# Kernel tuning notes

Hardware: AMD Instinct MI355X
Metric: run time of the kernel (lower is better)

The kernel has to match this reference:

```python
import jax, jax.numpy as jnp
import numpy as np

# ---- static config (mirrors Spectral2xDown.__init__) ----
B, C_IN, C_OUT = 2, 256, 256
H_HI, W_HI = 256, 512
H_LO, W_LO = 128, 256
LMAX = H_LO            # 128
MMAX = W_LO // 2 + 1   # 129
GROUPS = 32
EPS_GN = 1e-5


def _cc_nodes_weights(n):
    """Clenshaw-Curtis nodes x_j=cos(pi*j/(n-1)) and quadrature weights on [-1,1]
    (torch_harmonics 'equiangular' grid)."""
    N = n - 1
    tj = np.pi * np.arange(n) / N
    xj = np.cos(tj)
    ks = np.arange(1, N // 2 + 1)
    b = np.where(2 * ks == N, 1.0, 2.0)
    s = (b / (4.0 * ks**2 - 1.0))[None, :] * np.cos(2.0 * ks[None, :] * tj[:, None])
    w = (2.0 / N) * (1.0 - s.sum(axis=1))
    w[0] = w[-1] = (1.0 / N**2) if (N % 2) else (1.0 / (N**2 - 1.0))
    return xj, w


def _legpoly(mmax, lmax, x):
    """Orthonormal associated Legendre (-1)^m c_lm P_lm(x), shape [mmax,lmax,len(x)]
    (torch_harmonics _precompute_legpoly, norm='ortho', csphase=True)."""
    nmax = max(mmax, lmax)
    vdm = np.zeros((nmax, nmax, len(x)))
    vdm[0, 0] = 1.0 / np.sqrt(4.0 * np.pi)
    for l in range(1, nmax):
        vdm[l - 1, l] = np.sqrt(2 * l + 1) * x * vdm[l - 1, l - 1]
        vdm[l, l] = np.sqrt((2 * l + 1) * (1 + x) * (1 - x) / (2 * l)) * vdm[l - 1, l - 1]
    for l in range(2, nmax):
        for m in range(0, l - 1):
            vdm[m, l] = (x * np.sqrt((2 * l - 1) / (l - m) * (2 * l + 1) / (l + m)) * vdm[m, l - 1]
                         - np.sqrt((l + m - 1) / (l - m) * (2 * l + 1) / (2 * l - 3)
                                   * (l - m - 1) / (l + m)) * vdm[m, l - 2])
    vdm = vdm[:mmax, :lmax].copy()
    for m in range(1, mmax, 2):  # Condon-Shortley phase
        vdm[m] *= -1.0
    return vdm


def _precompute():
    ct_hi, w_hi = _cc_nodes_weights(H_HI)
    pct_hi = _legpoly(MMAX, LMAX, np.flip(np.arccos(ct_hi)) * 0 + np.cos(np.flip(np.arccos(ct_hi))))
    wmat_hi = pct_hi * w_hi[None, None, :]          # quadrature folded in: [M,L,K_hi]
    ct_lo, _ = _cc_nodes_weights(H_LO)
    pct_lo = _legpoly(MMAX, LMAX, np.cos(np.flip(np.arccos(ct_lo))))  # [M,L,K_lo]
    return wmat_hi.astype(np.float32), pct_lo.astype(np.float32)


def setup_inputs() -> dict:
    key = jax.random.key(0)
    k1, k2 = jax.random.split(key, 2)
    x = jax.random.normal(k1, (B, C_IN, H_HI, W_HI), jnp.float32)
    conv_w = jax.random.normal(k2, (C_OUT, C_IN), jnp.float32) / np.sqrt(C_IN)
    conv_b = jnp.zeros((C_OUT,), jnp.float32)
    gamma = jnp.ones((C_OUT,), jnp.float32)
    beta = jnp.zeros((C_OUT,), jnp.float32)
    wmat_hi, pct_lo = _precompute()
    return {"x": x, "conv_w": conv_w, "conv_b": conv_b, "gamma": gamma, "beta": beta,
            "wmat_hi": jnp.asarray(wmat_hi), "pct_lo": jnp.asarray(pct_lo)}


def reference(x, conv_w, conv_b, gamma, beta, wmat_hi, pct_lo):
    # --- forward real SHT on high-res grid (2*pi * rfft(norm='forward') + Legendre quadrature) ---
    X = (2.0 * jnp.pi / W_HI) * jnp.fft.rfft(x, axis=-1)     # [B,C,K_hi,W_HI//2+1]
    X = X[..., :MMAX]                                        # truncate to mmax
    flm_r = jnp.einsum('bckm,mlk->bclm', X.real, wmat_hi)    # [B,C,L,M]
    flm_i = jnp.einsum('bckm,mlk->bclm', X.imag, wmat_hi)
    # --- inverse real SHT on low-res grid ---
    g = (jnp.einsum('bclm,mlk->bckm', flm_r, pct_lo)
         + 1j * jnp.einsum('bclm,mlk->bckm', flm_i, pct_lo))  # [B,C,K_lo,M]
    y = jnp.fft.irfft(g, n=W_LO, axis=-1) * W_LO             # irfft norm='forward'
    # --- 1x1 conv -> GroupNorm(32) -> exact GELU ---
    h = jnp.einsum('bchw,oc->bohw', y, conv_w) + conv_b[None, :, None, None]
    hg = h.reshape(B, GROUPS, C_OUT // GROUPS, H_LO, W_LO)
    mu = hg.mean(axis=(2, 3, 4), keepdims=True)
    var = ((hg - mu) ** 2).mean(axis=(2, 3, 4), keepdims=True)
    hn = ((hg - mu) * jax.lax.rsqrt(var + EPS_GN)).reshape(B, C_OUT, H_LO, W_LO)
    out = hn * gamma[None, :, None, None] + beta[None, :, None, None]
    return jax.nn.gelu(out, approximate=False)
```

## Files before the change

### kernel.cpp

```cpp
#include <hip/hip_runtime.h>
#include <math.h>


#define ROWS_HI 131072
#define ROWS_LO 65536

#define B_FT    0LL
#define B_FIT   262144LL
#define B_WM    393216LL
#define B_PCT   8781824LL
#define B_WB    12976128LL
#define B_STATS 13107200LL
#define B_R1    13107712LL
#define B_R2    80216576LL

typedef __attribute__((ext_vector_type(8))) short bf16x8;
typedef __attribute__((ext_vector_type(8))) unsigned short ushort8;
typedef __attribute__((ext_vector_type(4))) unsigned short ushort4v;
typedef __attribute__((ext_vector_type(4))) float f32x4;

__device__ inline unsigned short f2bf(float f){
  unsigned int u = __float_as_uint(f);
  unsigned int r = u + 0x7FFFu + ((u >> 16) & 1u);
  return (unsigned short)(r >> 16);
}

__global__ __launch_bounds__(256) void k_tables(unsigned char* __restrict__ ws){
  unsigned short* FT  = (unsigned short*)(ws + B_FT);
  unsigned short* FIT = (unsigned short*)(ws + B_FIT);
  float* stats = (float*)(ws + B_STATS);
  int idx = blockIdx.x*256 + threadIdx.x;
  if (idx < 131072){
    int p = idx >> 9, w = idx & 511, m = p >> 1;
    int pr = (m*w) & 511;
    float ang = (float)pr * (float)(2.0*M_PI/512.0);
    float s, c; sincosf(ang, &s, &c);
    const float S = (float)(2.0*M_PI/512.0);
    FT[idx] = f2bf((p & 1) ? (-S*s) : (S*c));
  }
  int i2 = idx - 131072;
  if (i2 >= 0 && i2 < 65536){
    int w = i2 >> 8, p = i2 & 255, m = p >> 1;
    float eps = (m == 0) ? 1.f : 2.f;
    int pr = (m*w) & 255;
    float ang = (float)pr * (float)(2.0*M_PI/256.0);
    float s, c; sincosf(ang, &s, &c);
    FIT[i2] = f2bf((p & 1) ? (-eps*s) : (eps*c));
  }
  int i3 = idx - (131072 + 65536);
  if (i3 >= 0 && i3 < 128) stats[i3] = 0.f;
}

__global__ __launch_bounds__(256) void k_prep(const float* __restrict__ wmat,
                                              const float* __restrict__ pct,
                                              const float* __restrict__ Wc,
                                              unsigned char* __restrict__ ws){
  unsigned short* WM = (unsigned short*)(ws + B_WM);
  unsigned short* PT = (unsigned short*)(ws + B_PCT);
  unsigned short* WB = (unsigned short*)(ws + B_WB);
  int idx = blockIdx.x*256 + threadIdx.x;
  if (idx < 4194304){
    WM[idx] = f2bf(wmat[idx]);
  } else if (idx < 6291456){
    int j = idx - 4194304;
    int m = j >> 14, kp = (j >> 7) & 127, l = j & 127;
    PT[j] = f2bf(pct[m*16384 + l*128 + kp]);
  } else if (idx < 6356992){
    int j = idx - 6291456;
    WB[j] = f2bf(Wc[j]);
  }
}

template<int AMODE, int CMODE, bool BIAS, int MT, int NT, int SKIP>
__global__ __launch_bounds__(256) void k_gemm(
    const float* __restrict__ Af,
    const unsigned short* __restrict__ Abf,
    const unsigned short* __restrict__ Bt,
    float* __restrict__ Cf,
    unsigned short* __restrict__ Cbf,
    const float* __restrict__ bias,
    int ldA, int ldB, int ldC, int ksteps,
    long long sA, long long sB, int bzsh, long long sC)
{
  constexpr int BM = MT*32;
  constexpr int BN = NT*32;
  __shared__ unsigned short As[BM][40];
  __shared__ unsigned short Bs[BN][40];
  const int tid = threadIdx.x;
  const int z = blockIdx.z;
  const int m = z >> 1;
  const long long offA = (long long)z * sA;
  const long long offB = (long long)(z >> bzsh) * sB;
  const long long offC = (long long)z * sC;
  const int row0 = blockIdx.x * BM;
  const int n0   = blockIdx.y * BN;
  const int lane = tid & 63;
  const int wv = tid >> 6;
  const int wm = wv >> 1, wn = wv & 1;
  const int fr = lane & 15, q = lane >> 4;

  f32x4 acc[MT][NT];
#pragma unroll
  for (int i=0;i<MT;++i)
#pragma unroll
    for (int j=0;j<NT;++j) acc[i][j] = (f32x4){0.f,0.f,0.f,0.f};

  int ks0 = (SKIP == 2) ? (m >> 5) : 0;
  for (int ks = ks0; ks < ksteps; ++ks){
    const int k0 = ks * 32;
    if (AMODE == 0){
      const int row = tid >> 1, half = tid & 1;
      const float* s = Af + offA + (long long)(row0 + row) * ldA + k0 + half*16;
      float vv[16];
      *(float4*)(vv+0)  = *(const float4*)(s+0);
      *(float4*)(vv+4)  = *(const float4*)(s+4);
      *(float4*)(vv+8)  = *(const float4*)(s+8);
      *(float4*)(vv+12) = *(const float4*)(s+12);
      ushort8 H0, H1;
#pragma unroll
      for (int j=0;j<8;++j){ H0[j] = f2bf(vv[j]); H1[j] = f2bf(vv[8+j]); }
      *(ushort8*)&As[row][half*16]   = H0;
      *(ushort8*)&As[row][half*16+8] = H1;
    } else if (BM == 256){
      const unsigned short* s = Abf + offA + (long long)(row0 + tid) * ldA + k0;
      *(ushort8*)&As[tid][0]  = *(const ushort8*)(s);
      *(ushort8*)&As[tid][8]  = *(const ushort8*)(s+8);
      *(ushort8*)&As[tid][16] = *(const ushort8*)(s+16);
      *(ushort8*)&As[tid][24] = *(const ushort8*)(s+24);
    } else {
      const int row = tid >> 1, half = tid & 1;
      const unsigned short* s = Abf + offA + (long long)(row0 + row) * ldA + k0 + half*16;
      *(ushort8*)&As[row][half*16]   = *(const ushort8*)(s);
      *(ushort8*)&As[row][half*16+8] = *(const ushort8*)(s+8);
    }
    if (BN == 256){
      const unsigned short* s = Bt + offB + (long long)(n0 + tid) * ldB + k0;
      *(ushort8*)&Bs[tid][0]  = *(const ushort8*)(s);
      *(ushort8*)&Bs[tid][8]  = *(const ushort8*)(s+8);
      *(ushort8*)&Bs[tid][16] = *(const ushort8*)(s+16);
      *(ushort8*)&Bs[tid][24] = *(const ushort8*)(s+24);
    } else {
      const int row = tid >> 1, half = tid & 1;
      const unsigned short* s = Bt + offB + (long long)(n0 + row) * ldB + k0 + half*16;
      *(ushort8*)&Bs[row][half*16]   = *(const ushort8*)(s);
      *(ushort8*)&Bs[row][half*16+8] = *(const ushort8*)(s+8);
    }
    __syncthreads();
    bf16x8 ah[MT];
#pragma unroll
    for (int mt=0;mt<MT;++mt)
      ah[mt] = *(const bf16x8*)&As[wm*(MT*16)+mt*16+fr][q*8];
#pragma unroll
    for (int nt=0;nt<NT;++nt){
      if (SKIP == 1 && (wn*(NT*16) + nt*16 + 16 <= m)) continue;
      bf16x8 bb = *(const bf16x8*)&Bs[wn*(NT*16)+nt*16+fr][q*8];
#pragma unroll
      for (int mt=0;mt<MT;++mt)
        acc[mt][nt] = __builtin_amdgcn_mfma_f32_16x16x32_bf16(ah[mt], bb, acc[mt][nt], 0,0,0);
    }
    __syncthreads();
  }

  if (CMODE == 0){
#pragma unroll
    for (int mt=0;mt<MT;++mt){
      int row = row0 + wm*(MT*16) + mt*16 + q*4;
      float bv0=0.f,bv1=0.f,bv2=0.f,bv3=0.f;
      if (BIAS){ bv0=bias[row]; bv1=bias[row+1]; bv2=bias[row+2]; bv3=bias[row+3]; }
#pragma unroll
      for (int nt=0;nt<NT;++nt){
        int col = n0 + wn*(NT*16) + nt*16 + fr;
        float* dst = Cf + offC + (long long)row * ldC + col;
        dst[0]                = acc[mt][nt][0] + bv0;
        dst[(long long)ldC]   = acc[mt][nt][1] + bv1;
        dst[(long long)ldC*2] = acc[mt][nt][2] + bv2;
        dst[(long long)ldC*3] = acc[mt][nt][3] + bv3;
      }
    }
  } else if (CMODE == 1){
#pragma unroll
    for (int nt=0;nt<NT;++nt){
      int colp = n0 + wn*(NT*16) + nt*16 + fr;
#pragma unroll
      for (int mt=0;mt<MT;++mt){
        int rowb = row0 + wm*(MT*16) + mt*16 + q*4;
        ushort4v h;
        h[0] = f2bf(acc[mt][nt][0]);
        h[1] = f2bf(acc[mt][nt][1]);
        h[2] = f2bf(acc[mt][nt][2]);
        h[3] = f2bf(acc[mt][nt][3]);
        *(ushort4v*)&Cbf[offC + (long long)colp * ldC + rowb] = h;
      }
    }
  } else {
#pragma unroll
    for (int mt=0;mt<MT;++mt){
      int row = row0 + wm*(MT*16) + mt*16 + q*4;
#pragma unroll
      for (int nt=0;nt<NT;++nt){
        int col = n0 + wn*(NT*16) + nt*16 + fr;
        unsigned short* dst = Cbf + offC + (long long)row * ldC + col;
        dst[0]      = f2bf(acc[mt][nt][0]);
        dst[ldC]    = f2bf(acc[mt][nt][1]);
        dst[ldC*2]  = f2bf(acc[mt][nt][2]);
        dst[ldC*3]  = f2bf(acc[mt][nt][3]);
      }
    }
  }
}

__global__ __launch_bounds__(256) void k_trb(const unsigned short* __restrict__ g,
                                             unsigned short* __restrict__ gT){
  __shared__ unsigned short t[64][68];
  const int r0 = blockIdx.x * 64;
  const int p0 = blockIdx.y * 64;
  const int tr = threadIdx.x & 15, tc = threadIdx.x >> 4;
#pragma unroll
  for (int i=0;i<4;++i){
    int pl = tc + i*16;
    ushort4v v = *(const ushort4v*)(g + (long long)(p0+pl)*ROWS_LO + r0 + tr*4);
    *(ushort4v*)&t[pl][tr*4] = v;
  }
  __syncthreads();
#pragma unroll
  for (int i=0;i<4;++i){
    int rl = tc + i*16;
    ushort4v w;
    w[0]=t[tr*4+0][rl]; w[1]=t[tr*4+1][rl]; w[2]=t[tr*4+2][rl]; w[3]=t[tr*4+3][rl];
    *(ushort4v*)(gT + (long long)(r0+rl)*256 + p0 + tr*4) = w;
  }
}

__global__ __launch_bounds__(256) void k_tr2(const float* __restrict__ y,
                                             unsigned short* __restrict__ yT){
  __shared__ float t[64][65];
  const int s0 = blockIdx.x * 64;
  const int c0 = blockIdx.y * 64;
  const int b  = blockIdx.z;
  const int tr = threadIdx.x & 15, tc = threadIdx.x >> 4;
#pragma unroll
  for (int i=0;i<4;++i){
    int cl = tc + i*16;
    float4 v = *(const float4*)(y + (long long)b*8388608 + (long long)(c0+cl)*32768 + s0 + tr*4);
    t[cl][tr*4+0]=v.x; t[cl][tr*4+1]=v.y; t[cl][tr*4+2]=v.z; t[cl][tr*4+3]=v.w;
  }
  __syncthreads();
#pragma unroll
  for (int i=0;i<4;++i){
    int sl = tc + i*16;
    ushort4v w;
    w[0]=f2bf(t[tr*4+0][sl]); w[1]=f2bf(t[tr*4+1][sl]);
    w[2]=f2bf(t[tr*4+2][sl]); w[3]=f2bf(t[tr*4+3][sl]);
    *(ushort4v*)(yT + (long long)b*8388608 + (long long)(s0+sl)*256 + c0 + tr*4) = w;
  }
}

__global__ __launch_bounds__(256) void k_stats(const float* __restrict__ h,
                                               float* __restrict__ stats){
  const int bg = blockIdx.y;
  const int j  = blockIdx.x;
  const int t  = threadIdx.x;
  const float* base = h + (long long)bg*262144 + j*8192;
  float s = 0.f, ss = 0.f;
#pragma unroll
  for (int i=0;i<8;++i){
    float4 v = *(const float4*)(base + i*1024 + t*4);
    s  += v.x + v.y + v.z + v.w;
    ss += v.x*v.x + v.y*v.y + v.z*v.z + v.w*v.w;
  }
#pragma unroll
  for (int off=32; off>0; off>>=1){
    s  += __shfl_down(s, off, 64);
    ss += __shfl_down(ss, off, 64);
  }
  __shared__ float red[8];
  int wid = t >> 6;
  if ((t & 63) == 0){ red[wid*2] = s; red[wid*2+1] = ss; }
  __syncthreads();
  if (t == 0){
    float S  = red[0]+red[2]+red[4]+red[6];
    float SS = red[1]+red[3]+red[5]+red[7];
    atomicAdd(&stats[bg*2+0], S);
    atomicAdd(&stats[bg*2+1], SS);
  }
}

__global__ __launch_bounds__(256) void k_norm(float* __restrict__ out,
                                              const float* __restrict__ stats,
                                              const float* __restrict__ gamma,
                                              const float* __restrict__ beta){
  long long idx4 = ((long long)blockIdx.x*256 + threadIdx.x)*4;
  int o = (int)((idx4 >> 15) & 255);
  int b = (int)(idx4 >> 23);
  int bg = b*32 + (o >> 3);
  const float inv_n = 1.0f/262144.0f;
  float mean = stats[bg*2+0] * inv_n;
  float var  = stats[bg*2+1] * inv_n - mean*mean;
  float sc = rsqrtf(var + 1e-5f);
  float ga = gamma[o], be = beta[o];
  float4 v = *(float4*)(out + idx4);
  float t0 = (v.x - mean)*sc*ga + be;
  float t1 = (v.y - mean)*sc*ga + be;
  float t2 = (v.z - mean)*sc*ga + be;
  float t3 = (v.w - mean)*sc*ga + be;
  const float ISQ2 = 0.70710678118654752f;
  v.x = 0.5f*t0*(1.0f + erff(t0*ISQ2));
  v.y = 0.5f*t1*(1.0f + erff(t1*ISQ2));
  v.z = 0.5f*t2*(1.0f + erff(t2*ISQ2));
  v.w = 0.5f*t3*(1.0f + erff(t3*ISQ2));
  *(float4*)(out + idx4) = v;
}

extern "C" void kernel_launch(void* const* d_in, const int* in_sizes, int n_in,
                              void* d_out, int out_size, void* d_ws, size_t ws_size,
                              hipStream_t stream){
  const float* x      = (const float*)d_in[0];
  const float* conv_w = (const float*)d_in[1];
  const float* conv_b = (const float*)d_in[2];
  const float* gamma  = (const float*)d_in[3];
  const float* beta   = (const float*)d_in[4];
  const float* wmat   = (const float*)d_in[5];
  const float* pct    = (const float*)d_in[6];
  unsigned char* ws = (unsigned char*)d_ws;

  unsigned short* FT   = (unsigned short*)(ws + B_FT);
  unsigned short* FIT  = (unsigned short*)(ws + B_FIT);
  unsigned short* WM   = (unsigned short*)(ws + B_WM);
  unsigned short* PT   = (unsigned short*)(ws + B_PCT);
  unsigned short* WB   = (unsigned short*)(ws + B_WB);
  float*          stats= (float*)(ws + B_STATS);
  unsigned short* Xbf  = (unsigned short*)(ws + B_R1);
  unsigned short* gb   = (unsigned short*)(ws + B_R1);
  float*          y    = (float*)(ws + B_R1);
  unsigned short* flmb = (unsigned short*)(ws + B_R2);
  unsigned short* gTb  = (unsigned short*)(ws + B_R2);
  unsigned short* yT   = (unsigned short*)(ws + B_R2);
  float* out = (float*)d_out;

  k_tables<<<769, 256, 0, stream>>>(ws);
  k_prep  <<<24832, 256, 0, stream>>>(wmat, pct, conv_w, ws);

  k_gemm<0,1,false,4,8,0><<<dim3(1024,1,1), 256, 0, stream>>>(
      x, nullptr, FT, nullptr, Xbf, nullptr, 512, 512, ROWS_HI, 16, 0, 0, 0, 0);
  k_gemm<1,2,false,4,4,1><<<dim3(4,1,256), 256, 0, stream>>>(
      nullptr, Xbf, WM, nullptr, flmb, nullptr, 256, 256, 128, 8,
      131072LL, 32768LL, 1, 65536LL);
  k_gemm<1,2,false,4,4,2><<<dim3(4,1,256), 256, 0, stream>>>(
      nullptr, flmb, PT, nullptr, gb, nullptr, 128, 128, 128, 4,
      65536LL, 16384LL, 1, 65536LL);
  k_trb<<<dim3(1024,4), 256, 0, stream>>>(gb, gTb);
  k_gemm<1,0,false,4,8,0><<<dim3(512,1,1), 256, 0, stream>>>(
      nullptr, gTb, FIT, y, nullptr, nullptr, 256, 256, 256, 8, 0, 0, 0, 0);
  k_tr2<<<dim3(512,4,2), 256, 0, stream>>>(y, yT);
  k_gemm<1,0,true,8,4,0><<<dim3(1,256,2), 256, 0, stream>>>(
      nullptr, WB, yT, out, nullptr, conv_b, 256, 256, 32768, 8,
      0, 8388608LL, 0, 8388608LL);

  k_stats<<<dim3(32,64), 256, 0, stream>>>(out, stats);
  k_norm <<<16384, 256, 0, stream>>>(out, stats, gamma, beta);
}
```

Measured before the change: 670.5 us.

## Unify GEMM tiling to 128x128x64, fuse GroupNorm stats, store irfft output as bf16

All GEMMs now share one 128x128 tile with a 64-wide K step, replacing the earlier per-call tile shapes, and the launch grids are adjusted to match. The GroupNorm sum and sum-of-squares reduction moves into the epilogue of the 1x1-conv GEMM using wave shuffles and atomics, which removes the separate stats kernel and its extra read of the output. The inverse-FFT GEMM now writes bf16 directly, so the transpose kernel moves half the bytes. Costs are more atomics, a different occupancy profile from the larger LDS tiles with launch_bounds(256,3), and the stats epilogue assuming each 16-row fragment spans exactly two groups.

```diff
diff --git a/kernel.cpp b/kernel.cpp
--- a/kernel.cpp
+++ b/kernel.cpp
@@ -1,4 +1,5 @@
 #include <hip/hip_runtime.h>
+#include <hip/hip_bf16.h>
 #include <math.h>
 
 
@@ -23,6 +24,11 @@
   unsigned int u = __float_as_uint(f);
   unsigned int r = u + 0x7FFFu + ((u >> 16) & 1u);
   return (unsigned short)(r >> 16);
+}
+__device__ inline unsigned int pk2bf(float a, float b){
+  unsigned int lo = (unsigned int)f2bf(a);
+  unsigned int hi = (unsigned int)f2bf(b);
+  return lo | (hi << 16);
 }
 
 __global__ __launch_bounds__(256) void k_tables(unsigned char* __restrict__ ws){
@@ -71,134 +77,155 @@
   }
 }
 
-template<int AMODE, int CMODE, bool BIAS, int MT, int NT, int SKIP>
-__global__ __launch_bounds__(256) void k_gemm(
+template<int AMODE, int CMODE, bool BIAS, int SKIP, bool STATS>
+__global__ __launch_bounds__(256, 3) void k_gemm(
     const float* __restrict__ Af,
     const unsigned short* __restrict__ Abf,
     const unsigned short* __restrict__ Bt,
     float* __restrict__ Cf,
     unsigned short* __restrict__ Cbf,
     const float* __restrict__ bias,
+    float* __restrict__ stats,
     int ldA, int ldB, int ldC, int ksteps,
     long long sA, long long sB, int bzsh, long long sC)
 {
-  constexpr int BM = MT*32;
-  constexpr int BN = NT*32;
-  __shared__ unsigned short As[BM][40];
-  __shared__ unsigned short Bs[BN][40];
+  __shared__ unsigned short As[128][80];
+  __shared__ unsigned short Bs[128][80];
   const int tid = threadIdx.x;
   const int z = blockIdx.z;
   const int m = z >> 1;
   const long long offA = (long long)z * sA;
   const long long offB = (long long)(z >> bzsh) * sB;
   const long long offC = (long long)z * sC;
-  const int row0 = blockIdx.x * BM;
-  const int n0   = blockIdx.y * BN;
+  const int row0 = blockIdx.x * 128;
+  const int n0   = blockIdx.y * 128;
   const int lane = tid & 63;
   const int wv = tid >> 6;
   const int wm = wv >> 1, wn = wv & 1;
   const int fr = lane & 15, q = lane >> 4;
-
-  f32x4 acc[MT][NT];
-#pragma unroll
-  for (int i=0;i<MT;++i)
-#pragma unroll
-    for (int j=0;j<NT;++j) acc[i][j] = (f32x4){0.f,0.f,0.f,0.f};
-
-  int ks0 = (SKIP == 2) ? (m >> 5) : 0;
+  const int srow = tid >> 1, shalf = tid & 1;
+
+  f32x4 acc[4][4];
+#pragma unroll
+  for (int i=0;i<4;++i)
+#pragma unroll
+    for (int j=0;j<4;++j) acc[i][j] = (f32x4){0.f,0.f,0.f,0.f};
+
+  const int ks0 = (SKIP == 2) ? (m >> 6) : 0;
   for (int ks = ks0; ks < ksteps; ++ks){
-    const int k0 = ks * 32;
+    const int k0 = ks * 64;
     if (AMODE == 0){
-      const int row = tid >> 1, half = tid & 1;
-      const float* s = Af + offA + (long long)(row0 + row) * ldA + k0 + half*16;
-      float vv[16];
-      *(float4*)(vv+0)  = *(const float4*)(s+0);
-      *(float4*)(vv+4)  = *(const float4*)(s+4);
-      *(float4*)(vv+8)  = *(const float4*)(s+8);
-      *(float4*)(vv+12) = *(const float4*)(s+12);
-      ushort8 H0, H1;
-#pragma unroll
-      for (int j=0;j<8;++j){ H0[j] = f2bf(vv[j]); H1[j] = f2bf(vv[8+j]); }
-      *(ushort8*)&As[row][half*16]   = H0;
-      *(ushort8*)&As[row][half*16+8] = H1;
-    } else if (BM == 256){
-      const unsigned short* s = Abf + offA + (long long)(row0 + tid) * ldA + k0;
-      *(ushort8*)&As[tid][0]  = *(const ushort8*)(s);
-      *(ushort8*)&As[tid][8]  = *(const ushort8*)(s+8);
-      *(ushort8*)&As[tid][16] = *(const ushort8*)(s+16);
-      *(ushort8*)&As[tid][24] = *(const ushort8*)(s+24);
+      const float* s = Af + offA + (long long)(row0 + srow) * ldA + k0 + shalf*32;
+#pragma unroll
+      for (int b2=0;b2<2;++b2){
+        float4 v0 = *(const float4*)(s + b2*16 + 0);
+        float4 v1 = *(const float4*)(s + b2*16 + 4);
+        float4 v2 = *(const float4*)(s + b2*16 + 8);
+        float4 v3 = *(const float4*)(s + b2*16 + 12);
+        unsigned int u0 = pk2bf(v0.x, v0.y), u1 = pk2bf(v0.z, v0.w);
+        unsigned int u2 = pk2bf(v1.x, v1.y), u3 = pk2bf(v1.z, v1.w);
+        unsigned int u4 = pk2bf(v2.x, v2.y), u5 = pk2bf(v2.z, v2.w);
+        unsigned int u6 = pk2bf(v3.x, v3.y), u7 = pk2bf(v3.z, v3.w);
+        unsigned int* d = (unsigned int*)&As[srow][shalf*32 + b2*16];
+        d[0]=u0; d[1]=u1; d[2]=u2; d[3]=u3; d[4]=u4; d[5]=u5; d[6]=u6; d[7]=u7;
+      }
     } else {
-      const int row = tid >> 1, half = tid & 1;
-      const unsigned short* s = Abf + offA + (long long)(row0 + row) * ldA + k0 + half*16;
-      *(ushort8*)&As[row][half*16]   = *(const ushort8*)(s);
-      *(ushort8*)&As[row][half*16+8] = *(const ushort8*)(s+8);
-    }
-    if (BN == 256){
-      const unsigned short* s = Bt + offB + (long long)(n0 + tid) * ldB + k0;
-      *(ushort8*)&Bs[tid][0]  = *(const ushort8*)(s);
-      *(ushort8*)&Bs[tid][8]  = *(const ushort8*)(s+8);
-      *(ushort8*)&Bs[tid][16] = *(const ushort8*)(s+16);
-      *(ushort8*)&Bs[tid][24] = *(const ushort8*)(s+24);
-    } else {
-      const int row = tid >> 1, half = tid & 1;
-      const unsigned short* s = Bt + offB + (long long)(n0 + row) * ldB + k0 + half*16;
-      *(ushort8*)&Bs[row][half*16]   = *(const ushort8*)(s);
-      *(ushort8*)&Bs[row][half*16+8] = *(const ushort8*)(s+8);
+      const unsigned short* s = Abf + offA + (long long)(row0 + srow) * ldA + k0 + shalf*32;
+      *(ushort8*)&As[srow][shalf*32]    = *(const ushort8*)(s);
+      *(ushort8*)&As[srow][shalf*32+8]  = *(const ushort8*)(s+8);
+      *(ushort8*)&As[srow][shalf*32+16] = *(const ushort8*)(s+16);
+      *(ushort8*)&As[srow][shalf*32+24] = *(const ushort8*)(s+24);
+    }
+    {
+      const unsigned short* s = Bt + offB + (long long)(n0 + srow) * ldB + k0 + shalf*32;
+      *(ushort8*)&Bs[srow][shalf*32]    = *(const ushort8*)(s);
+      *(ushort8*)&Bs[srow][shalf*32+8]  = *(const ushort8*)(s+8);
+      *(ushort8*)&Bs[srow][shalf*32+16] = *(const ushort8*)(s+16);
+      *(ushort8*)&Bs[srow][shalf*32+24] = *(const ushort8*)(s+24);
     }
     __syncthreads();
-    bf16x8 ah[MT];
-#pragma unroll
-    for (int mt=0;mt<MT;++mt)
-      ah[mt] = *(const bf16x8*)&As[wm*(MT*16)+mt*16+fr][q*8];
-#pragma unroll
-    for (int nt=0;nt<NT;++nt){
-      if (SKIP == 1 && (wn*(NT*16) + nt*16 + 16 <= m)) continue;
-      bf16x8 bb = *(const bf16x8*)&Bs[wn*(NT*16)+nt*16+fr][q*8];
-#pragma unroll
-      for (int mt=0;mt<MT;++mt)
-        acc[mt][nt] = __builtin_amdgcn_mfma_f32_16x16x32_bf16(ah[mt], bb, acc[mt][nt], 0,0,0);
+#pragma unroll
+    for (int c=0;c<2;++c){
+      bf16x8 ah[4];
+#pragma unroll
+      for (int mt=0;mt<4;++mt)
+        ah[mt] = *(const bf16x8*)&As[wm*64+mt*16+fr][c*32 + q*8];
+#pragma unroll
+      for (int nt=0;nt<4;++nt){
+        if (SKIP == 1 && (wn*64 + nt*16 + 16 <= m)) continue;
+        bf16x8 bb = *(const bf16x8*)&Bs[wn*64+nt*16+fr][c*32 + q*8];
+#pragma unroll
+        for (int mt=0;mt<4;++mt)
+          acc[mt][nt] = __builtin_amdgcn_mfma_f32_16x16x32_bf16(ah[mt], bb, acc[mt][nt], 0,0,0);
+      }
     }
     __syncthreads();
   }
 
   if (CMODE == 0){
 #pragma unroll
-    for (int mt=0;mt<MT;++mt){
-      int row = row0 + wm*(MT*16) + mt*16 + q*4;
+    for (int mt=0;mt<4;++mt){
+      int row = row0 + wm*64 + mt*16 + q*4;
       float bv0=0.f,bv1=0.f,bv2=0.f,bv3=0.f;
       if (BIAS){ bv0=bias[row]; bv1=bias[row+1]; bv2=bias[row+2]; bv3=bias[row+3]; }
-#pragma unroll
-      for (int nt=0;nt<NT;++nt){
-        int col = n0 + wn*(NT*16) + nt*16 + fr;
+      float s_ = 0.f, ss_ = 0.f;
+#pragma unroll
+      for (int nt=0;nt<4;++nt){
+        int col = n0 + wn*64 + nt*16 + fr;
         float* dst = Cf + offC + (long long)row * ldC + col;
-        dst[0]                = acc[mt][nt][0] + bv0;
-        dst[(long long)ldC]   = acc[mt][nt][1] + bv1;
-        dst[(long long)ldC*2] = acc[mt][nt][2] + bv2;
-        dst[(long long)ldC*3] = acc[mt][nt][3] + bv3;
+        float v0 = acc[mt][nt][0] + bv0;
+        float v1 = acc[mt][nt][1] + bv1;
+        float v2 = acc[mt][nt][2] + bv2;
+        float v3 = acc[mt][nt][3] + bv3;
+        dst[0]                = v0;
+        dst[(long long)ldC]   = v1;
+        dst[(long long)ldC*2] = v2;
+        dst[(long long)ldC*3] = v3;
+        if (STATS){
+          s_  += v0 + v1 + v2 + v3;
+          ss_ += v0*v0 + v1*v1 + v2*v2 + v3*v3;
+        }
+      }
+      if (STATS){
+        float sl = (q < 2) ? s_ : 0.f, sh = (q < 2) ? 0.f : s_;
+        float ql = (q < 2) ? ss_ : 0.f, qh = (q < 2) ? 0.f : ss_;
+#pragma unroll
+        for (int off=32; off>0; off>>=1){
+          sl += __shfl_down(sl, off, 64);
+          sh += __shfl_down(sh, off, 64);
+          ql += __shfl_down(ql, off, 64);
+          qh += __shfl_down(qh, off, 64);
+        }
+        if (lane == 0){
+          int gb = (row0 + wm*64 + mt*16) >> 3;
+          int bg0 = z*32 + gb;
+          atomicAdd(&stats[bg0*2+0], sl);
+          atomicAdd(&stats[bg0*2+1], ql);
+          atomicAdd(&stats[(bg0+1)*2+0], sh);
+          atomicAdd(&stats[(bg0+1)*2+1], qh);
+        }
       }
     }
   } else if (CMODE == 1){
 #pragma unroll
-    for (int nt=0;nt<NT;++nt){
-      int colp = n0 + wn*(NT*16) + nt*16 + fr;
-#pragma unroll
-      for (int mt=0;mt<MT;++mt){
-        int rowb = row0 + wm*(MT*16) + mt*16 + q*4;
-        ushort4v h;
-        h[0] = f2bf(acc[mt][nt][0]);
-        h[1] = f2bf(acc[mt][nt][1]);
-        h[2] = f2bf(acc[mt][nt][2]);
-        h[3] = f2bf(acc[mt][nt][3]);
-        *(ushort4v*)&Cbf[offC + (long long)colp * ldC + rowb] = h;
+    for (int nt=0;nt<4;++nt){
+      int colp = n0 + wn*64 + nt*16 + fr;
+#pragma unroll
+      for (int mt=0;mt<4;++mt){
+        int rowb = row0 + wm*64 + mt*16 + q*4;
+        unsigned int u0 = pk2bf(acc[mt][nt][0], acc[mt][nt][1]);
+        unsigned int u1 = pk2bf(acc[mt][nt][2], acc[mt][nt][3]);
+        unsigned int* d = (unsigned int*)&Cbf[offC + (long long)colp * ldC + rowb];
+        d[0] = u0; d[1] = u1;
       }
     }
   } else {
 #pragma unroll
-    for (int mt=0;mt<MT;++mt){
-      int row = row0 + wm*(MT*16) + mt*16 + q*4;
-#pragma unroll
-      for (int nt=0;nt<NT;++nt){
-        int col = n0 + wn*(NT*16) + nt*16 + fr;
+    for (int mt=0;mt<4;++mt){
+      int row = row0 + wm*64 + mt*16 + q*4;
+#pragma unroll
+      for (int nt=0;nt<4;++nt){
+        int col = n0 + wn*64 + nt*16 + fr;
         unsigned short* dst = Cbf + offC + (long long)row * ldC + col;
         dst[0]      = f2bf(acc[mt][nt][0]);
         dst[ldC]    = f2bf(acc[mt][nt][1]);
@@ -231,9 +258,9 @@
   }
 }
 
-__global__ __launch_bounds__(256) void k_tr2(const float* __restrict__ y,
-                                             unsigned short* __restrict__ yT){
-  __shared__ float t[64][65];
+__global__ __launch_bounds__(256) void k_tr2b(const unsigned short* __restrict__ y,
+                                              unsigned short* __restrict__ yT){
+  __shared__ unsigned short t[64][68];
   const int s0 = blockIdx.x * 64;
   const int c0 = blockIdx.y * 64;
   const int b  = blockIdx.z;
@@ -241,47 +268,16 @@
 #pragma unroll
   for (int i=0;i<4;++i){
     int cl = tc + i*16;
-    float4 v = *(const float4*)(y + (long long)b*8388608 + (long long)(c0+cl)*32768 + s0 + tr*4);
-    t[cl][tr*4+0]=v.x; t[cl][tr*4+1]=v.y; t[cl][tr*4+2]=v.z; t[cl][tr*4+3]=v.w;
+    ushort4v v = *(const ushort4v*)(y + (long long)b*8388608 + (long long)(c0+cl)*32768 + s0 + tr*4);
+    *(ushort4v*)&t[cl][tr*4] = v;
   }
   __syncthreads();
 #pragma unroll
   for (int i=0;i<4;++i){
     int sl = tc + i*16;
     ushort4v w;
-    w[0]=f2bf(t[tr*4+0][sl]); w[1]=f2bf(t[tr*4+1][sl]);
-    w[2]=f2bf(t[tr*4+2][sl]); w[3]=f2bf(t[tr*4+3][sl]);
+    w[0]=t[tr*4+0][sl]; w[1]=t[tr*4+1][sl]; w[2]=t[tr*4+2][sl]; w[3]=t[tr*4+3][sl];
     *(ushort4v*)(yT + (long long)b*8388608 + (long long)(s0+sl)*256 + c0 + tr*4) = w;
-  }
-}
-
-__global__ __launch_bounds__(256) void k_stats(const float* __restrict__ h,
-                                               float* __restrict__ stats){
-  const int bg = blockIdx.y;
-  const int j  = blockIdx.x;
-  const int t  = threadIdx.x;
-  const float* base = h + (long long)bg*262144 + j*8192;
-  float s = 0.f, ss = 0.f;
-#pragma unroll
-  for (int i=0;i<8;++i){
-    float4 v = *(const float4*)(base + i*1024 + t*4);
-    s  += v.x + v.y + v.z + v.w;
-    ss += v.x*v.x + v.y*v.y + v.z*v.z + v.w*v.w;
-  }
-#pragma unroll
-  for (int off=32; off>0; off>>=1){
-    s  += __shfl_down(s, off, 64);
-    ss += __shfl_down(ss, off, 64);
-  }
-  __shared__ float red[8];
-  int wid = t >> 6;
-  if ((t & 63) == 0){ red[wid*2] = s; red[wid*2+1] = ss; }
-  __syncthreads();
-  if (t == 0){
-    float S  = red[0]+red[2]+red[4]+red[6];
-    float SS = red[1]+red[3]+red[5]+red[7];
-    atomicAdd(&stats[bg*2+0], S);
-    atomicAdd(&stats[bg*2+1], SS);
   }
 }
 
@@ -331,7 +327,7 @@
   float*          stats= (float*)(ws + B_STATS);
   unsigned short* Xbf  = (unsigned short*)(ws + B_R1);
   unsigned short* gb   = (unsigned short*)(ws + B_R1);
-  float*          y    = (float*)(ws + B_R1);
+  unsigned short* ybf  = (unsigned short*)(ws + B_R1);
   unsigned short* flmb = (unsigned short*)(ws + B_R2);
   unsigned short* gTb  = (unsigned short*)(ws + B_R2);
   unsigned short* yT   = (unsigned short*)(ws + B_R2);
@@ -340,22 +336,21 @@
   k_tables<<<769, 256, 0, stream>>>(ws);
   k_prep  <<<24832, 256, 0, stream>>>(wmat, pct, conv_w, ws);
 
-  k_gemm<0,1,false,4,8,0><<<dim3(1024,1,1), 256, 0, stream>>>(
-      x, nullptr, FT, nullptr, Xbf, nullptr, 512, 512, ROWS_HI, 16, 0, 0, 0, 0);
-  k_gemm<1,2,false,4,4,1><<<dim3(4,1,256), 256, 0, stream>>>(
-      nullptr, Xbf, WM, nullptr, flmb, nullptr, 256, 256, 128, 8,
+  k_gemm<0,1,false,0,false><<<dim3(1024,2,1), 256, 0, stream>>>(
+      x, nullptr, FT, nullptr, Xbf, nullptr, nullptr, 512, 512, ROWS_HI, 8, 0, 0, 0, 0);
+  k_gemm<1,2,false,1,false><<<dim3(4,1,256), 256, 0, stream>>>(
+      nullptr, Xbf, WM, nullptr, flmb, nullptr, nullptr, 256, 256, 128, 4,
       131072LL, 32768LL, 1, 65536LL);
-  k_gemm<1,2,false,4,4,2><<<dim3(4,1,256), 256, 0, stream>>>(
-      nullptr, flmb, PT, nullptr, gb, nullptr, 128, 128, 128, 4,
+  k_gemm<1,2,false,2,false><<<dim3(4,1,256), 256, 0, stream>>>(
+      nullptr, flmb, PT, nullptr, gb, nullptr, nullptr, 128, 128, 128, 2,
       65536LL, 16384LL, 1, 65536LL);
   k_trb<<<dim3(1024,4), 256, 0, stream>>>(gb, gTb);
-  k_gemm<1,0,false,4,8,0><<<dim3(512,1,1), 256, 0, stream>>>(
-      nullptr, gTb, FIT, y, nullptr, nullptr, 256, 256, 256, 8, 0, 0, 0, 0);
-  k_tr2<<<dim3(512,4,2), 256, 0, stream>>>(y, yT);
-  k_gemm<1,0,true,8,4,0><<<dim3(1,256,2), 256, 0, stream>>>(
-      nullptr, WB, yT, out, nullptr, conv_b, 256, 256, 32768, 8,
+  k_gemm<1,2,false,0,false><<<dim3(512,2,1), 256, 0, stream>>>(
+      nullptr, gTb, FIT, nullptr, ybf, nullptr, nullptr, 256, 256, 256, 4, 0, 0, 0, 0);
+  k_tr2b<<<dim3(512,4,2), 256, 0, stream>>>(ybf, yT);
+  k_gemm<1,0,true,0,true><<<dim3(2,256,2), 256, 0, stream>>>(
+      nullptr, WB, yT, out, nullptr, conv_b, stats, 256, 256, 32768, 4,
       0, 8388608LL, 0, 8388608LL);
 
-  k_stats<<<dim3(32,64), 256, 0, stream>>>(out, stats);
   k_norm <<<16384, 256, 0, stream>>>(out, stats, gamma, beta);
 }
```

Measured after the change: 891.5 us. 33.0% more time.
